# Kernel tuning notes

Hardware: AMD Instinct MI355X
Metric: run time of the kernel (lower is better)

The kernel has to match this reference:

```python
import jax, jax.numpy as jnp
import numpy as np

# DeformConv hyperparameters (from init_kwargs)
KH, KW = 3, 3
STRIDE, PAD, DIL = 1, 1, 1
GROUPS, DG = 1, 1  # groups=1, deformable_groups=1
B, C, H, W = 4, 64, 128, 128
O = 64
HO = (H + 2 * PAD - (DIL * (KH - 1) + 1)) // STRIDE + 1  # 128
WO = (W + 2 * PAD - (DIL * (KW - 1) + 1)) // STRIDE + 1  # 128


def setup_inputs() -> dict:
    key = jax.random.key(0)
    k1, k2, k3, k4 = jax.random.split(key, 4)
    x = jax.random.normal(k1, (B, C, H, W), dtype=jnp.float32)
    # offset channels: dg * K * 2, ordered (y, x) per kernel tap (DCNv1 CUDA layout)
    offset = jax.random.normal(k2, (B, 2 * DG * KH * KW, HO, WO), dtype=jnp.float32)
    fan_in = C * KH * KW
    weight = jax.random.normal(k3, (O, C // GROUPS, KH, KW), dtype=jnp.float32) / np.sqrt(fan_in)
    bias = jax.random.normal(k4, (O,), dtype=jnp.float32) * 0.01
    return {"x": x, "offset": offset, "weight": weight, "bias": bias}


def _deform_sample(x, offset):
    """Bilinear-sample x at deformed kernel tap locations.
    Returns [B, C, K, HO, WO] where K = KH*KW."""
    K = KH * KW
    Cg = C // DG
    # offset -> [B, DG, K, 2, HO, WO]; channel layout: dg*2*K, pairs (y, x)
    off = offset.reshape(B, DG, K, 2, HO, WO)
    off_y, off_x = off[:, :, :, 0], off[:, :, :, 1]  # [B, DG, K, HO, WO]

    ki = (jnp.arange(K) // KW).astype(jnp.float32)  # kernel row
    kj = (jnp.arange(K) % KW).astype(jnp.float32)   # kernel col
    base_h = (jnp.arange(HO) * STRIDE - PAD).astype(jnp.float32)
    base_w = (jnp.arange(WO) * STRIDE - PAD).astype(jnp.float32)

    # sampling positions [B, DG, K, HO, WO]
    py = off_y + (ki * DIL)[None, None, :, None, None] + base_h[None, None, None, :, None]
    px = off_x + (kj * DIL)[None, None, :, None, None] + base_w[None, None, None, None, :]

    y0f = jnp.floor(py)
    x0f = jnp.floor(px)
    ly = py - y0f
    lx = px - x0f
    hy = 1.0 - ly
    hx = 1.0 - lx
    y0 = y0f.astype(jnp.int32)
    x0 = x0f.astype(jnp.int32)
    y1 = y0 + 1
    x1 = x0 + 1

    flat = x.reshape(B, DG, Cg, H * W)

    def gather(yi, xi, wgt):
        valid = (yi >= 0) & (yi < H) & (xi >= 0) & (xi < W)
        idx = jnp.clip(yi, 0, H - 1) * W + jnp.clip(xi, 0, W - 1)
        idx = idx.reshape(B, DG, 1, K * HO * WO)
        v = jnp.take_along_axis(flat, idx, axis=-1).reshape(B, DG, Cg, K, HO, WO)
        return v * (wgt * valid.astype(wgt.dtype))[:, :, None]

    val = (gather(y0, x0, hy * hx) + gather(y0, x1, hy * lx)
           + gather(y1, x0, ly * hx) + gather(y1, x1, ly * lx))
    return val.reshape(B, C, K, HO, WO)


def reference(x, offset, weight, bias):
    sampled = _deform_sample(x, offset)              # [B, C, K, HO, WO]
    w = weight.reshape(O, C, KH * KW)                # groups = 1
    out = jnp.einsum('bckhw,ock->bohw', sampled, w)  # im2col + GEMM
    return out + bias[None, :, None, None]
```

## Files before the change

kernel.cpp:

```cpp
#include <hip/hip_runtime.h>
#include <hip/hip_fp16.h>


#define B_  4
#define C_  64
#define H_  128
#define W_  128
#define O_  64
#define HO_ 128
#define WO_ 128
#define NCHUNK 8
#define NGW 12
#define KSTEPS 3
#define NT_ 32
#define NTASK (9 * NT_)
#define SG  10
#define SBUF (SG * NT_ * 8)
#define TR  16
#define TC  48
#define TSLOTS (TR * TC)

typedef _Float16 half8 __attribute__((ext_vector_type(8)));
typedef __attribute__((ext_vector_type(4))) float f32x4;

union H8 { float4 v; __half2 h2[4]; half8 v8; };

__global__ __launch_bounds__(256)
void prep(const float* __restrict__ x, const float* __restrict__ w,
          __half* __restrict__ xt, __half* __restrict__ wt) {
    const int tid = threadIdx.x;
    if (blockIdx.x < 2048) {
        int t = blockIdx.x * 256 + tid;
        int xc = t & 127;
        int y  = (t >> 7) & 127;
        int ch = (t >> 14) & 7;
        int b  = t >> 17;
        const float* xp = x + (((size_t)(b * C_ + ch * 8) * H_) + y) * W_ + xc;
        union { __half h[8]; float4 v; } pk;
#pragma unroll
        for (int e = 0; e < 8; ++e) pk.h[e] = __float2half_rn(xp[e * H_ * W_]);
        *(float4*)(xt + (size_t)t * 8) = pk.v;
    } else {
        int t = (blockIdx.x - 2048) * 256 + tid;
        if (t >= NCHUNK * NGW * O_) return;
        int o  = t & 63;
        int g  = (t >> 6) % NGW;
        int ch = (t >> 6) / NGW;
        union { __half h[8]; float4 v; } pk;
#pragma unroll
        for (int e = 0; e < 8; ++e)
            pk.h[e] = (g < 9) ? __float2half_rn(w[(o * C_ + ch * 8 + e) * 9 + g])
                              : __half(0.0f);
        *(float4*)(wt + (size_t)t * 8) = pk.v;
    }
}

__global__ __launch_bounds__(256, 4)
void dcn_mfma(const __half* __restrict__ xt, const float* __restrict__ off,
              const __half* __restrict__ wt, const float* __restrict__ bias,
              float* __restrict__ out) {
    __shared__ __align__(16) _Float16 sS[2 * SBUF];
    __shared__ __align__(16) _Float16 sT[TSLOTS * 8];

    const int tid = threadIdx.x;
    const int bid = blockIdx.x;
    const int w4  = bid & 3;
    const int ho  = (bid >> 2) & (HO_ - 1);
    const int b   = bid >> 9;
    const int woB = w4 * NT_;
    const int yb  = ho - 7;
    const int xb  = woB - 8;

    int ty0_[2], ty1_[2], tx_[2], fb_[2];
    __half2 ua2_[2], ub2_[2], va2_[2], vb2_[2];
#pragma unroll
    for (int r = 0; r < 2; ++r) {
        int task = tid + r * 256;
        int tk = (task < NTASK) ? task : 0;
        int k  = tk >> 5;
        int wo = (tk & (NT_ - 1)) + woB;
        int ki = k / 3, kj = k - 3 * ki;
        float oy = off[(((b * 18) + 2 * k    ) * HO_ + ho) * WO_ + wo];
        float ox = off[(((b * 18) + 2 * k + 1) * HO_ + ho) * WO_ + wo];
        float py = (float)(ho - 1 + ki) + oy;
        float px = (float)(wo - 1 + kj) + ox;
        float y0f = floorf(py), x0f = floorf(px);
        int   y0 = (int)y0f,   x0 = (int)x0f;
        float ly = py - y0f,   lx = px - x0f;
        float hy = 1.f - ly,   hx = 1.f - lx;
        int y1 = y0 + 1, x1 = x0 + 1;
        float vy0 = (y0 >= 0 && y0 < H_) ? 1.f : 0.f;
        float vy1 = (y1 >= 0 && y1 < H_) ? 1.f : 0.f;
        float vx0 = (x0 >= 0 && x0 < W_) ? 1.f : 0.f;
        float vx1 = (x1 >= 0 && x1 < W_) ? 1.f : 0.f;
        int cy0 = min(max(y0, 0), H_ - 1), cy1 = min(max(y1, 0), H_ - 1);
        int cx0 = min(max(x0, 0), W_ - 1), cx1 = min(max(x1, 0), W_ - 1);
        int ax  = min(max(x0, 0), W_ - 2);
        float w00 = hy * hx * vy0 * vx0;
        float w01 = hy * lx * vy0 * vx1;
        float w10 = ly * hx * vy1 * vx0;
        float w11 = ly * lx * vy1 * vx1;
        float s0 = (cx0 != ax) ? 1.f : 0.f;
        float s1 = (cx1 != ax) ? 1.f : 0.f;
        ty0_[r] = cy0 - yb;
        ty1_[r] = cy1 - yb;
        tx_[r]  = ax - xb;
        fb_[r]  = ((unsigned)ty0_[r] > (unsigned)(TR - 1)) |
                  ((unsigned)ty1_[r] > (unsigned)(TR - 1)) |
                  ((unsigned)tx_[r]  > (unsigned)(TC - 2));
        ua2_[r] = __float2half2_rn(w00 * (1.f - s0) + w01 * (1.f - s1));
        ub2_[r] = __float2half2_rn(w00 * s0 + w01 * s1);
        va2_[r] = __float2half2_rn(w10 * (1.f - s0) + w11 * (1.f - s1));
        vb2_[r] = __float2half2_rn(w10 * s0 + w11 * s1);
    }

    int gofs[3];
#pragma unroll
    for (int j = 0; j < 3; ++j) {
        int s  = tid + j * 256;
        int rr = s / TC, cc = s - rr * TC;
        int yc = min(max(yb + rr, 0), H_ - 1);
        int xc = min(max(xb + cc, 0), W_ - 1);
        gofs[j] = yc * W_ + xc;
    }

    if (tid < 128) {
        ((unsigned int*)&sS[9 * NT_ * 8])[tid]        = 0u;
        ((unsigned int*)&sS[SBUF + 9 * NT_ * 8])[tid] = 0u;
    }

    float4 pf0, pf1, pf2;
    auto issue = [&](int ch) {
        const float4* xc = (const float4*)(xt + ((size_t)(b * NCHUNK + ch)) * (H_ * W_ * 8));
        pf0 = xc[gofs[0]];
        pf1 = xc[gofs[1]];
        pf2 = xc[gofs[2]];
    };

    auto sample = [&](int ch) {
        _Float16* buf = sS + (ch & 1) * SBUF;
        const float4* xcg = (const float4*)(xt + ((size_t)(b * NCHUNK + ch)) * (H_ * W_ * 8));
        const float4* tl  = (const float4*)sT;
#pragma unroll
        for (int r = 0; r < 2; ++r) {
            int task = tid + r * 256;
            if (task < NTASK) {
                int k  = task >> 5;
                int wo = task & (NT_ - 1);
                H8 q00, q01, q10, q11;
                if (!fb_[r]) {
                    int a0 = ty0_[r] * TC + tx_[r];
                    int a1 = ty1_[r] * TC + tx_[r];
                    q00.v = tl[a0];  q01.v = tl[a0 + 1];
                    q10.v = tl[a1];  q11.v = tl[a1 + 1];
                } else {
                    int a0 = (ty0_[r] + yb) * W_ + (tx_[r] + xb);
                    int a1 = (ty1_[r] + yb) * W_ + (tx_[r] + xb);
                    q00.v = xcg[a0]; q01.v = xcg[a0 + 1];
                    q10.v = xcg[a1]; q11.v = xcg[a1 + 1];
                }
                H8 s;
#pragma unroll
                for (int j = 0; j < 4; ++j) {
                    __half2 t0 = __hmul2(ua2_[r], q00.h2[j]);
                    t0 = __hfma2(ub2_[r], q01.h2[j], t0);
                    t0 = __hfma2(va2_[r], q10.h2[j], t0);
                    t0 = __hfma2(vb2_[r], q11.h2[j], t0);
                    s.h2[j] = t0;
                }
                *(half8*)&buf[(k * NT_ + wo) * 8] = s.v8;
            }
        }
    };

    const int lane = tid & 63;
    const int wv   = tid >> 6;
    const int ow   = wv & 1;
    const int nw   = wv >> 1;
    const int quad = lane >> 4;
    const int l15  = lane & 15;

    f32x4 acc[2];
    acc[0] = (f32x4){0.f, 0.f, 0.f, 0.f};
    acc[1] = (f32x4){0.f, 0.f, 0.f, 0.f};

    auto mfma_chunk = [&](int ch) {
        const __half*   wc  = wt + (size_t)(ch * NGW) * O_ * 8;
        const _Float16* buf = sS + (ch & 1) * SBUF;
#pragma unroll
        for (int ks = 0; ks < KSTEPS; ++ks) {
            int g  = ks * 4 + quad;
            int gb = (g < 9) ? g : 9;
            half8 bfr = *(const half8*)&buf[(gb * NT_ + nw * 16 + l15) * 8];
#pragma unroll
            for (int ot = 0; ot < 2; ++ot) {
                half8 afr = *(const half8*)(wc + (size_t)(g * O_ + ow * 32 + ot * 16 + l15) * 8);
                acc[ot] = __builtin_amdgcn_mfma_f32_16x16x32_f16(afr, bfr, acc[ot], 0, 0, 0);
            }
        }
    };

    issue(0);
    for (int ch = 0; ch < NCHUNK; ++ch) {
        float4* tw = (float4*)sT;
        tw[tid]       = pf0;
        tw[tid + 256] = pf1;
        tw[tid + 512] = pf2;
        __syncthreads();
        if (ch + 1 < NCHUNK) issue(ch + 1);
        sample(ch);
        if (ch > 0) mfma_chunk(ch - 1);
        __syncthreads();
    }
    mfma_chunk(NCHUNK - 1);

#pragma unroll
    for (int ot = 0; ot < 2; ++ot) {
        int wo = woB + nw * 16 + l15;
#pragma unroll
        for (int rg = 0; rg < 4; ++rg) {
            int o = ow * 32 + ot * 16 + quad * 4 + rg;
            out[(((size_t)(b * O_ + o)) * HO_ + ho) * WO_ + wo] = acc[ot][rg] + bias[o];
        }
    }
}

extern "C" void kernel_launch(void* const* d_in, const int* in_sizes, int n_in,
                              void* d_out, int out_size, void* d_ws, size_t ws_size,
                              hipStream_t stream) {
    const float* x    = (const float*)d_in[0];
    const float* off  = (const float*)d_in[1];
    const float* w    = (const float*)d_in[2];
    const float* bias = (const float*)d_in[3];
    float* out = (float*)d_out;

    __half* wt = (__half*)d_ws;
    __half* xt = (__half*)((char*)d_ws + 262144);

    hipLaunchKernelGGL(prep, dim3(2048 + 24), dim3(256), 0, stream, x, w, xt, wt);
    hipLaunchKernelGGL(dcn_mfma, dim3(B_ * HO_ * (WO_ / NT_)), dim3(256), 0, stream,
                       xt, off, wt, bias, out);
}
```

Before: 99.30 us.

## Process two output rows per block to reuse staged input tile and weights

```diff
diff --git a/kernel.cpp b/kernel.cpp
--- a/kernel.cpp
+++ b/kernel.cpp
@@ -13,9 +13,11 @@
 #define NGW 12
 #define KSTEPS 3
 #define NT_ 32
-#define NTASK (9 * NT_)
+#define NROW 2
+#define NCOL 64
+#define NTASK (9 * NCOL)
 #define SG  10
-#define SBUF (SG * NT_ * 8)
+#define SBUF (SG * NCOL * 8)
 #define TR  16
 #define TC  48
 #define TSLOTS (TR * TC)
@@ -65,53 +67,59 @@
     const int tid = threadIdx.x;
     const int bid = blockIdx.x;
     const int w4  = bid & 3;
-    const int ho  = (bid >> 2) & (HO_ - 1);
-    const int b   = bid >> 9;
+    const int hp  = (bid >> 2) & 63;
+    const int b   = bid >> 8;
+    const int ho  = hp << 1;
     const int woB = w4 * NT_;
-    const int yb  = ho - 7;
+    const int yb  = ho - 6;
     const int xb  = woB - 8;
 
-    int ty0_[2], ty1_[2], tx_[2], fb_[2];
-    __half2 ua2_[2], ub2_[2], va2_[2], vb2_[2];
-#pragma unroll
-    for (int r = 0; r < 2; ++r) {
-        int task = tid + r * 256;
-        int tk = (task < NTASK) ? task : 0;
-        int k  = tk >> 5;
-        int wo = (tk & (NT_ - 1)) + woB;
-        int ki = k / 3, kj = k - 3 * ki;
-        float oy = off[(((b * 18) + 2 * k    ) * HO_ + ho) * WO_ + wo];
-        float ox = off[(((b * 18) + 2 * k + 1) * HO_ + ho) * WO_ + wo];
-        float py = (float)(ho - 1 + ki) + oy;
-        float px = (float)(wo - 1 + kj) + ox;
-        float y0f = floorf(py), x0f = floorf(px);
-        int   y0 = (int)y0f,   x0 = (int)x0f;
-        float ly = py - y0f,   lx = px - x0f;
-        float hy = 1.f - ly,   hx = 1.f - lx;
-        int y1 = y0 + 1, x1 = x0 + 1;
-        float vy0 = (y0 >= 0 && y0 < H_) ? 1.f : 0.f;
-        float vy1 = (y1 >= 0 && y1 < H_) ? 1.f : 0.f;
-        float vx0 = (x0 >= 0 && x0 < W_) ? 1.f : 0.f;
-        float vx1 = (x1 >= 0 && x1 < W_) ? 1.f : 0.f;
-        int cy0 = min(max(y0, 0), H_ - 1), cy1 = min(max(y1, 0), H_ - 1);
-        int cx0 = min(max(x0, 0), W_ - 1), cx1 = min(max(x1, 0), W_ - 1);
-        int ax  = min(max(x0, 0), W_ - 2);
-        float w00 = hy * hx * vy0 * vx0;
-        float w01 = hy * lx * vy0 * vx1;
-        float w10 = ly * hx * vy1 * vx0;
-        float w11 = ly * lx * vy1 * vx1;
-        float s0 = (cx0 != ax) ? 1.f : 0.f;
-        float s1 = (cx1 != ax) ? 1.f : 0.f;
-        ty0_[r] = cy0 - yb;
-        ty1_[r] = cy1 - yb;
-        tx_[r]  = ax - xb;
-        fb_[r]  = ((unsigned)ty0_[r] > (unsigned)(TR - 1)) |
-                  ((unsigned)ty1_[r] > (unsigned)(TR - 1)) |
-                  ((unsigned)tx_[r]  > (unsigned)(TC - 2));
-        ua2_[r] = __float2half2_rn(w00 * (1.f - s0) + w01 * (1.f - s1));
-        ub2_[r] = __float2half2_rn(w00 * s0 + w01 * s1);
-        va2_[r] = __float2half2_rn(w10 * (1.f - s0) + w11 * (1.f - s1));
-        vb2_[r] = __float2half2_rn(w10 * s0 + w11 * s1);
+    int a0_[3], a1_[3], nf_[3];
+    __half2 ua2_[3], ub2_[3], va2_[3], vb2_[3];
+#pragma unroll
+    for (int r = 0; r < 3; ++r) {
+        bool act = (r < 2) || ((tid & 3) == 0);
+        if (act) {
+            int task = (r < 2) ? (tid + r * 256) : (512 + (tid >> 2));
+            int k  = task >> 6;
+            int n  = task & 63;
+            int wo = (n & 31) + woB;
+            int hr = ho + (n >> 5);
+            int ki = k / 3, kj = k - 3 * ki;
+            float oy = off[(((b * 18) + 2 * k    ) * HO_ + hr) * WO_ + wo];
+            float ox = off[(((b * 18) + 2 * k + 1) * HO_ + hr) * WO_ + wo];
+            float py = (float)(hr - 1 + ki) + oy;
+            float px = (float)(wo - 1 + kj) + ox;
+            float y0f = floorf(py), x0f = floorf(px);
+            int   y0 = (int)y0f,   x0 = (int)x0f;
+            float ly = py - y0f,   lx = px - x0f;
+            float hy = 1.f - ly,   hx = 1.f - lx;
+            int y1 = y0 + 1, x1 = x0 + 1;
+            float vy0 = (y0 >= 0 && y0 < H_) ? 1.f : 0.f;
+            float vy1 = (y1 >= 0 && y1 < H_) ? 1.f : 0.f;
+            float vx0 = (x0 >= 0 && x0 < W_) ? 1.f : 0.f;
+            float vx1 = (x1 >= 0 && x1 < W_) ? 1.f : 0.f;
+            int cy0 = min(max(y0, 0), H_ - 1), cy1 = min(max(y1, 0), H_ - 1);
+            int ax  = min(max(x0, 0), W_ - 2);
+            int cx0 = min(max(x0, 0), W_ - 1), cx1 = min(max(x1, 0), W_ - 1);
+            float w00 = hy * hx * vy0 * vx0;
+            float w01 = hy * lx * vy0 * vx1;
+            float w10 = ly * hx * vy1 * vx0;
+            float w11 = ly * lx * vy1 * vx1;
+            float s0 = (cx0 != ax) ? 1.f : 0.f;
+            float s1 = (cx1 != ax) ? 1.f : 0.f;
+            int t0 = cy0 - yb, t1 = cy1 - yb, txx = ax - xb;
+            int fb = ((unsigned)t0  > (TR - 1)) |
+                     ((unsigned)t1  > (TR - 1)) |
+                     ((unsigned)txx > (TC - 2));
+            nf_[r] = !fb;
+            a0_[r] = fb ? (cy0 * W_ + ax) : (t0 * TC + txx);
+            a1_[r] = fb ? (cy1 * W_ + ax) : (t1 * TC + txx);
+            ua2_[r] = __float2half2_rn(w00 * (1.f - s0) + w01 * (1.f - s1));
+            ub2_[r] = __float2half2_rn(w00 * s0 + w01 * s1);
+            va2_[r] = __float2half2_rn(w10 * (1.f - s0) + w11 * (1.f - s1));
+            vb2_[r] = __float2half2_rn(w10 * s0 + w11 * s1);
+        }
     }
 
     int gofs[3];
@@ -124,10 +132,8 @@
         gofs[j] = yc * W_ + xc;
     }
 
-    if (tid < 128) {
-        ((unsigned int*)&sS[9 * NT_ * 8])[tid]        = 0u;
-        ((unsigned int*)&sS[SBUF + 9 * NT_ * 8])[tid] = 0u;
-    }
+    ((unsigned int*)&sS[9 * NCOL * 8])[tid]        = 0u;
+    ((unsigned int*)&sS[SBUF + 9 * NCOL * 8])[tid] = 0u;
 
     float4 pf0, pf1, pf2;
     auto issue = [&](int ch) {
@@ -142,20 +148,18 @@
         const float4* xcg = (const float4*)(xt + ((size_t)(b * NCHUNK + ch)) * (H_ * W_ * 8));
         const float4* tl  = (const float4*)sT;
 #pragma unroll
-        for (int r = 0; r < 2; ++r) {
-            int task = tid + r * 256;
-            if (task < NTASK) {
-                int k  = task >> 5;
-                int wo = task & (NT_ - 1);
+        for (int r = 0; r < 3; ++r) {
+            bool act = (r < 2) || ((tid & 3) == 0);
+            if (act) {
+                int task = (r < 2) ? (tid + r * 256) : (512 + (tid >> 2));
+                int k = task >> 6;
+                int n = task & 63;
+                int a0 = a0_[r], a1 = a1_[r];
                 H8 q00, q01, q10, q11;
-                if (!fb_[r]) {
-                    int a0 = ty0_[r] * TC + tx_[r];
-                    int a1 = ty1_[r] * TC + tx_[r];
+                if (nf_[r]) {
                     q00.v = tl[a0];  q01.v = tl[a0 + 1];
                     q10.v = tl[a1];  q11.v = tl[a1 + 1];
                 } else {
-                    int a0 = (ty0_[r] + yb) * W_ + (tx_[r] + xb);
-                    int a1 = (ty1_[r] + yb) * W_ + (tx_[r] + xb);
                     q00.v = xcg[a0]; q01.v = xcg[a0 + 1];
                     q10.v = xcg[a1]; q11.v = xcg[a1 + 1];
                 }
@@ -168,7 +172,7 @@
                     t0 = __hfma2(vb2_[r], q11.h2[j], t0);
                     s.h2[j] = t0;
                 }
-                *(half8*)&buf[(k * NT_ + wo) * 8] = s.v8;
+                *(half8*)&buf[(k * NCOL + n) * 8] = s.v8;
             }
         }
     };
@@ -180,9 +184,12 @@
     const int quad = lane >> 4;
     const int l15  = lane & 15;
 
-    f32x4 acc[2];
-    acc[0] = (f32x4){0.f, 0.f, 0.f, 0.f};
-    acc[1] = (f32x4){0.f, 0.f, 0.f, 0.f};
+    f32x4 acc[2][2];
+#pragma unroll
+    for (int ot = 0; ot < 2; ++ot)
+#pragma unroll
+        for (int nt = 0; nt < 2; ++nt)
+            acc[ot][nt] = (f32x4){0.f, 0.f, 0.f, 0.f};
 
     auto mfma_chunk = [&](int ch) {
         const __half*   wc  = wt + (size_t)(ch * NGW) * O_ * 8;
@@ -191,11 +198,13 @@
         for (int ks = 0; ks < KSTEPS; ++ks) {
             int g  = ks * 4 + quad;
             int gb = (g < 9) ? g : 9;
-            half8 bfr = *(const half8*)&buf[(gb * NT_ + nw * 16 + l15) * 8];
+            half8 bfr0 = *(const half8*)&buf[(gb * NCOL + nw * 32 +      l15) * 8];
+            half8 bfr1 = *(const half8*)&buf[(gb * NCOL + nw * 32 + 16 + l15) * 8];
 #pragma unroll
             for (int ot = 0; ot < 2; ++ot) {
                 half8 afr = *(const half8*)(wc + (size_t)(g * O_ + ow * 32 + ot * 16 + l15) * 8);
-                acc[ot] = __builtin_amdgcn_mfma_f32_16x16x32_f16(afr, bfr, acc[ot], 0, 0, 0);
+                acc[ot][0] = __builtin_amdgcn_mfma_f32_16x16x32_f16(afr, bfr0, acc[ot][0], 0, 0, 0);
+                acc[ot][1] = __builtin_amdgcn_mfma_f32_16x16x32_f16(afr, bfr1, acc[ot][1], 0, 0, 0);
             }
         }
     };
@@ -216,11 +225,17 @@
 
 #pragma unroll
     for (int ot = 0; ot < 2; ++ot) {
-        int wo = woB + nw * 16 + l15;
-#pragma unroll
-        for (int rg = 0; rg < 4; ++rg) {
-            int o = ow * 32 + ot * 16 + quad * 4 + rg;
-            out[(((size_t)(b * O_ + o)) * HO_ + ho) * WO_ + wo] = acc[ot][rg] + bias[o];
+#pragma unroll
+        for (int nt = 0; nt < 2; ++nt) {
+            int n   = nw * 32 + nt * 16 + l15;
+            int row = n >> 5;
+            int wo  = woB + (n & 31);
+#pragma unroll
+            for (int rg = 0; rg < 4; ++rg) {
+                int o = ow * 32 + ot * 16 + quad * 4 + rg;
+                out[(((size_t)(b * O_ + o)) * HO_ + ho + row) * WO_ + wo] =
+                    acc[ot][nt][rg] + bias[o];
+            }
         }
     }
 }
@@ -238,6 +253,6 @@
     __half* xt = (__half*)((char*)d_ws + 262144);
 
     hipLaunchKernelGGL(prep, dim3(2048 + 24), dim3(256), 0, stream, x, w, xt, wt);
-    hipLaunchKernelGGL(dcn_mfma, dim3(B_ * HO_ * (WO_ / NT_)), dim3(256), 0, stream,
+    hipLaunchKernelGGL(dcn_mfma, dim3(B_ * (HO_ / NROW) * (WO_ / NT_)), dim3(256), 0, stream,
                        xt, off, wt, bias, out);
 }
```

Result: faster. 96.74 us (-2.6%).
